# Kernel tuning notes

Measured on AMD Instinct MI355X. Metric: run time of the kernel, lower is better.

The kernel has to match this reference:

```python
import jax, jax.numpy as jnp
import numpy as np
import math

N, E = 50000, 800000
HID, EDIM, H = 128, 32, 8
D = HID // H            # head_dim = 16
FFN = 4 * HID           # ModelConstants.FFN_EXPANSION_FACTOR = 4
EPS = 1e-5


def layer_norm(x, g, b):
    mu = jnp.mean(x, axis=-1, keepdims=True)
    var = jnp.var(x, axis=-1, keepdims=True)
    return (x - mu) * jax.lax.rsqrt(var + EPS) * g + b


def setup_inputs() -> dict:
    key = jax.random.key(0)
    ks = jax.random.split(key, 16)
    s = 1.0 / math.sqrt(HID)
    inp = {
        "x": jax.random.normal(ks[0], (N, HID), jnp.float32),
        "edge_index": jax.random.randint(ks[1], (2, E), 0, N, jnp.int32),
        "edge_attr": jax.random.normal(ks[2], (E, EDIM), jnp.float32),
        # projections stored as (in, out): y = x @ W + b (same math as torch Linear)
        "qW": jax.random.normal(ks[3], (HID, HID), jnp.float32) * s,
        "qb": jnp.zeros((HID,), jnp.float32),
        "kW": jax.random.normal(ks[4], (HID, HID), jnp.float32) * s,
        "kb": jnp.zeros((HID,), jnp.float32),
        "vW": jax.random.normal(ks[5], (HID, HID), jnp.float32) * s,
        "vb": jnp.zeros((HID,), jnp.float32),
        "eW": jax.random.normal(ks[6], (EDIM, H), jnp.float32) / math.sqrt(EDIM),
        "eb": jnp.zeros((H,), jnp.float32),
        "oW": jax.random.normal(ks[7], (HID, HID), jnp.float32) * s,
        "ob": jnp.zeros((HID,), jnp.float32),
        "ln1_g": jnp.ones((HID,), jnp.float32),
        "ln1_b": jnp.zeros((HID,), jnp.float32),
        "f1W": jax.random.normal(ks[8], (HID, FFN), jnp.float32) * s,
        "f1b": jnp.zeros((FFN,), jnp.float32),
        "lnf_g": jnp.ones((FFN,), jnp.float32),
        "lnf_b": jnp.zeros((FFN,), jnp.float32),
        "f2W": jax.random.normal(ks[9], (FFN, HID), jnp.float32) / math.sqrt(FFN),
        "f2b": jnp.zeros((HID,), jnp.float32),
        "ln2_g": jnp.ones((HID,), jnp.float32),
        "ln2_b": jnp.zeros((HID,), jnp.float32),
    }
    return inp


def reference(x, edge_index, edge_attr, qW, qb, kW, kb, vW, vb, eW, eb, oW, ob,
              ln1_g, ln1_b, f1W, f1b, lnf_g, lnf_b, f2W, f2b, ln2_g, ln2_b):
    src, dst = edge_index[0], edge_index[1]
    q = (x @ qW + qb).reshape(N, H, D)
    k = (x @ kW + kb).reshape(N, H, D)
    v = (x @ vW + vb).reshape(N, H, D)
    edge_bias = edge_attr @ eW + eb                     # (E, H)
    # per-edge attention scores
    scores = jnp.sum(q[src] * k[dst], axis=-1) / math.sqrt(D) + edge_bias  # (E, H)
    # scatter softmax over edges grouped by dst
    mx = jax.ops.segment_max(scores, dst, num_segments=N)  # (N, H), -inf for empty
    mx = jnp.where(jnp.isinf(mx), jnp.zeros_like(mx), mx)
    ex = jnp.exp(scores - mx[dst])                      # (E, H)
    den = jax.ops.segment_sum(ex, dst, num_segments=N)
    den = jnp.maximum(den, 1e-8)
    attn = ex / den[dst]                                # (E, H)
    # weighted aggregation
    wv = v[src] * attn[:, :, None]                      # (E, H, D)
    out = jax.ops.segment_sum(wv, dst, num_segments=N)  # (N, H, D)
    out = out.reshape(N, HID) @ oW + ob
    x = layer_norm(x + out, ln1_g, ln1_b)
    h = x @ f1W + f1b
    h = jax.nn.gelu(layer_norm(h, lnf_g, lnf_b), approximate=False)
    h = h @ f2W + f2b
    x = layer_norm(x + h, ln2_g, ln2_b)
    return x
```

## Files before the change

### kernel.cpp

```cpp
#include <hip/hip_runtime.h>
#include <math.h>

#define LN_EPS 1e-5f

typedef __attribute__((ext_vector_type(8))) __bf16 bf16x8;
typedef __attribute__((ext_vector_type(4))) float f32x4;

__device__ inline float bf2f(unsigned short u) {
  union { unsigned int i; float f; } x; x.i = ((unsigned int)u) << 16; return x.f;
}
__device__ inline unsigned short f2bf(float f) {
  union { float f; unsigned int i; } x; x.f = f;
  unsigned int r = (x.i + 0x7FFFu + ((x.i >> 16) & 1u)) >> 16;
  return (unsigned short)r;
}
__device__ inline void gload_lds16(const void* g, void* l) {
  __builtin_amdgcn_global_load_lds((const __attribute__((address_space(1))) void*)g,
                                   (__attribute__((address_space(3))) void*)l, 16, 0, 0);
}

__global__ __launch_bounds__(256)
void to_bf16(const float* __restrict__ in, unsigned short* __restrict__ outp, long n) {
  long i = ((long)blockIdx.x * 256 + threadIdx.x) * 4;
  if (i >= n) return;
  float4 v = *(const float4*)&in[i];
  ushort4 o = { f2bf(v.x), f2bf(v.y), f2bf(v.z), f2bf(v.w) };
  *(ushort4*)&outp[i] = o;
}

__global__ __launch_bounds__(256)
void transpose_w(const float* __restrict__ W, unsigned short* __restrict__ Wt, int K, int M) {
  __shared__ float t[32][33];
  const int k0 = blockIdx.x * 32, m0 = blockIdx.y * 32;
  const int tx = threadIdx.x & 31, ty = threadIdx.x >> 5;
#pragma unroll
  for (int i = 0; i < 32; i += 8)
    t[ty + i][tx] = W[(size_t)(k0 + ty + i) * M + m0 + tx];
  __syncthreads();
#pragma unroll
  for (int i = 0; i < 32; i += 8)
    Wt[(size_t)(m0 + ty + i) * K + k0 + tx] = f2bf(t[tx][ty + i]);
}

__global__ __launch_bounds__(384)
void concat_bias3(const float* __restrict__ a, const float* __restrict__ b,
                  const float* __restrict__ c, float* __restrict__ o) {
  int t = threadIdx.x;
  o[t] = t < 128 ? a[t] : (t < 256 ? b[t - 128] : c[t - 256]);
}

template<bool OBF>
__global__ __launch_bounds__(256)
void gemm_mfma(const unsigned short* __restrict__ A, const unsigned short* __restrict__ Wt,
               const float* __restrict__ bias, void* __restrict__ Cout,
               int Nr, int K, int M) {
  __shared__ __align__(16) unsigned short As[128 * 64];
  __shared__ __align__(16) unsigned short Bs[128 * 64];
  const int tid = threadIdx.x;
  const int bm = blockIdx.x * 128, bn = blockIdx.y * 128;
  const int lane = tid & 63;
  const int wr = (tid >> 6) >> 1, wc = (tid >> 6) & 1;
  f32x4 acc[4][4] = {};
  const int nkt = K >> 6;
  for (int kt = 0; kt < nkt; ++kt) {
#pragma unroll
    for (int i = 0; i < 4; ++i) {
      int c = tid + i * 256;
      int row = c >> 3;
      int j = (c & 7) ^ (row & 7);
      int ar = bm + row; ar = ar < Nr ? ar : Nr - 1;
      gload_lds16(A + (size_t)ar * K + kt * 64 + j * 8, As + (size_t)c * 8);
      gload_lds16(Wt + (size_t)(bn + row) * K + kt * 64 + j * 8, Bs + (size_t)c * 8);
    }
    __syncthreads();
#pragma unroll
    for (int ks = 0; ks < 2; ++ks) {
      bf16x8 af[4], bfr[4];
#pragma unroll
      for (int f = 0; f < 4; ++f) {
        int rowa = wr * 64 + f * 16 + (lane & 15);
        int ja = (ks * 4 + (lane >> 4)) ^ (rowa & 7);
        af[f] = *(const bf16x8*)(As + rowa * 64 + ja * 8);
        int rowb = wc * 64 + f * 16 + (lane & 15);
        int jb = (ks * 4 + (lane >> 4)) ^ (rowb & 7);
        bfr[f] = *(const bf16x8*)(Bs + rowb * 64 + jb * 8);
      }
#pragma unroll
      for (int fr = 0; fr < 4; ++fr)
#pragma unroll
        for (int fc = 0; fc < 4; ++fc)
          acc[fr][fc] = __builtin_amdgcn_mfma_f32_16x16x32_bf16(af[fr], bfr[fc], acc[fr][fc], 0, 0, 0);
    }
    __syncthreads();
  }
#pragma unroll
  for (int fr = 0; fr < 4; ++fr) {
#pragma unroll
    for (int j = 0; j < 4; ++j) {
      int row = bm + wr * 64 + fr * 16 + (lane >> 4) * 4 + j;
      if (row < Nr) {
#pragma unroll
        for (int fc = 0; fc < 4; ++fc) {
          int col = bn + wc * 64 + fc * 16 + (lane & 15);
          float v = acc[fr][fc][j] + bias[col];
          if (OBF) ((unsigned short*)Cout)[(size_t)row * M + col] = f2bf(v);
          else     ((float*)Cout)[(size_t)row * M + col] = v;
        }
      }
    }
  }
}

template<bool WBF>
__global__ __launch_bounds__(256)
void gemm_ln(const unsigned short* __restrict__ A, const unsigned short* __restrict__ Wt,
             const float* __restrict__ bias, const float* __restrict__ res,
             const float* __restrict__ g, const float* __restrict__ b,
             float* __restrict__ y, unsigned short* __restrict__ ybf, int Nr, int K) {
  __shared__ __align__(16) unsigned short As[128 * 64];
  __shared__ __align__(16) unsigned short Bs[128 * 64];
  __shared__ float pls[128][2], plss[128][2];
  const int tid = threadIdx.x;
  const int bm = blockIdx.x * 128;
  const int lane = tid & 63;
  const int wr = (tid >> 6) >> 1, wc = (tid >> 6) & 1;
  f32x4 acc[4][4] = {};
  const int nkt = K >> 6;
  for (int kt = 0; kt < nkt; ++kt) {
#pragma unroll
    for (int i = 0; i < 4; ++i) {
      int c = tid + i * 256;
      int row = c >> 3;
      int j = (c & 7) ^ (row & 7);
      int ar = bm + row; ar = ar < Nr ? ar : Nr - 1;
      gload_lds16(A + (size_t)ar * K + kt * 64 + j * 8, As + (size_t)c * 8);
      gload_lds16(Wt + (size_t)row * K + kt * 64 + j * 8, Bs + (size_t)c * 8);
    }
    __syncthreads();
#pragma unroll
    for (int ks = 0; ks < 2; ++ks) {
      bf16x8 af[4], bfr[4];
#pragma unroll
      for (int f = 0; f < 4; ++f) {
        int rowa = wr * 64 + f * 16 + (lane & 15);
        int ja = (ks * 4 + (lane >> 4)) ^ (rowa & 7);
        af[f] = *(const bf16x8*)(As + rowa * 64 + ja * 8);
        int rowb = wc * 64 + f * 16 + (lane & 15);
        int jb = (ks * 4 + (lane >> 4)) ^ (rowb & 7);
        bfr[f] = *(const bf16x8*)(Bs + rowb * 64 + jb * 8);
      }
#pragma unroll
      for (int fr = 0; fr < 4; ++fr)
#pragma unroll
        for (int fc = 0; fc < 4; ++fc)
          acc[fr][fc] = __builtin_amdgcn_mfma_f32_16x16x32_bf16(af[fr], bfr[fc], acc[fr][fc], 0, 0, 0);
    }
    __syncthreads();
  }
#pragma unroll
  for (int fr = 0; fr < 4; ++fr) {
#pragma unroll
    for (int j = 0; j < 4; ++j) {
      const int rl = wr * 64 + fr * 16 + (lane >> 4) * 4 + j;
      const int row = bm + rl;
      const int rowc = row < Nr ? row : Nr - 1;
      float s = 0.f, ss = 0.f;
#pragma unroll
      for (int fc = 0; fc < 4; ++fc) {
        int col = wc * 64 + fc * 16 + (lane & 15);
        float val = acc[fr][fc][j] + bias[col] + res[(size_t)rowc * 128 + col];
        acc[fr][fc][j] = val;
        s += val; ss += val * val;
      }
      s += __shfl_xor(s, 1); ss += __shfl_xor(ss, 1);
      s += __shfl_xor(s, 2); ss += __shfl_xor(ss, 2);
      s += __shfl_xor(s, 4); ss += __shfl_xor(ss, 4);
      s += __shfl_xor(s, 8); ss += __shfl_xor(ss, 8);
      if ((lane & 15) == 0) { pls[rl][wc] = s; plss[rl][wc] = ss; }
    }
  }
  __syncthreads();
#pragma unroll
  for (int fr = 0; fr < 4; ++fr) {
#pragma unroll
    for (int j = 0; j < 4; ++j) {
      const int rl = wr * 64 + fr * 16 + (lane >> 4) * 4 + j;
      const int row = bm + rl;
      if (row >= Nr) continue;
      const float S = pls[rl][0] + pls[rl][1];
      const float SS = plss[rl][0] + plss[rl][1];
      const float mu = S * (1.f / 128.f);
      const float inv = rsqrtf(SS * (1.f / 128.f) - mu * mu + LN_EPS);
#pragma unroll
      for (int fc = 0; fc < 4; ++fc) {
        int col = wc * 64 + fc * 16 + (lane & 15);
        float o = (acc[fr][fc][j] - mu) * inv * g[col] + b[col];
        y[(size_t)row * 128 + col] = o;
        if (WBF) ybf[(size_t)row * 128 + col] = f2bf(o);
      }
    }
  }
}

__global__ __launch_bounds__(256)
void edge_hist(const int* __restrict__ ei, int* __restrict__ deg, int E) {
  int e = blockIdx.x * 256 + threadIdx.x;
  if (e < E) atomicAdd(&deg[ei[E + e]], 1);
}

__global__ __launch_bounds__(256)
void deg_block_sum(const int* __restrict__ deg, int* __restrict__ bsum, int N) {
  const int t = threadIdx.x;
  const int beg = blockIdx.x * 2048 + t * 8;
  int s = 0;
#pragma unroll
  for (int j = 0; j < 8; ++j) { int i = beg + j; if (i < N) s += deg[i]; }
#pragma unroll
  for (int off = 32; off; off >>= 1) s += __shfl_xor(s, off);
  __shared__ int ws[4];
  if ((t & 63) == 0) ws[t >> 6] = s;
  __syncthreads();
  if (t == 0) bsum[blockIdx.x] = ws[0] + ws[1] + ws[2] + ws[3];
}

__global__ __launch_bounds__(64)
void scan_bsum(int* __restrict__ bsum, int* __restrict__ offs_last, int nb) {
  const int t = threadIdx.x;
  int v = (t < nb) ? bsum[t] : 0;
  int inc = v;
#pragma unroll
  for (int off = 1; off < 64; off <<= 1) {
    int x = __shfl_up(inc, off);
    if (t >= off) inc += x;
  }
  if (t < nb) bsum[t] = inc - v;
  if (t == 63) *offs_last = inc;
}

__global__ __launch_bounds__(256)
void deg_scan_write(const int* __restrict__ deg, const int* __restrict__ bsum,
                    int* __restrict__ offs, int* __restrict__ pos, int N) {
  const int t = threadIdx.x;
  const int beg = blockIdx.x * 2048 + t * 8;
  int loc[8]; int T = 0;
#pragma unroll
  for (int j = 0; j < 8; ++j) { int i = beg + j; loc[j] = (i < N) ? deg[i] : 0; T += loc[j]; }
  int inc = T;
#pragma unroll
  for (int off = 1; off < 64; off <<= 1) {
    int x = __shfl_up(inc, off);
    if ((t & 63) >= off) inc += x;
  }
  __shared__ int ws[4];
  if ((t & 63) == 63) ws[t >> 6] = inc;
  __syncthreads();
  const int wid = t >> 6;
  int wbase = 0;
  for (int w = 0; w < wid; ++w) wbase += ws[w];
  int base = bsum[blockIdx.x] + wbase + inc - T;
#pragma unroll
  for (int j = 0; j < 8; ++j) {
    int i = beg + j;
    if (i < N) { offs[i] = base; pos[i] = base; base += loc[j]; }
  }
}

__global__ __launch_bounds__(256)
void edge_scatter_bias(const int* __restrict__ ei, int* __restrict__ pos,
                       const float* __restrict__ ea, const float* __restrict__ eW,
                       const float* __restrict__ eb, int* __restrict__ csr_src,
                       unsigned short* __restrict__ ebp, int E) {
  __shared__ float ews[256];
  __shared__ float ebs[8];
  const int tid = threadIdx.x;
  if (tid < 256) ews[tid] = eW[tid];
  if (tid < 8) ebs[tid] = eb[tid];
  __syncthreads();
  int e = blockIdx.x * 256 + tid;
  if (e >= E) return;
  float bias[8];
#pragma unroll
  for (int h = 0; h < 8; ++h) bias[h] = ebs[h];
#pragma unroll
  for (int i4 = 0; i4 < 8; ++i4) {
    float4 a = *(const float4*)&ea[(size_t)e * 32 + i4 * 4];
    float av[4] = {a.x, a.y, a.z, a.w};
#pragma unroll
    for (int j = 0; j < 4; ++j)
#pragma unroll
      for (int h = 0; h < 8; ++h) bias[h] += av[j] * ews[(i4 * 4 + j) * 8 + h];
  }
  int d = ei[E + e];
  int p = atomicAdd(&pos[d], 1);
  csr_src[p] = ei[e];
  union { unsigned short us[8]; uint4 v; } pk;
#pragma unroll
  for (int h = 0; h < 8; ++h) pk.us[h] = f2bf(bias[h]);
  *(uint4*)&ebp[(size_t)p * 8] = pk.v;
}

__global__ __launch_bounds__(256)
void node_agg(const int* __restrict__ csr_src, const int* __restrict__ offs,
              const unsigned short* __restrict__ qkv, const unsigned short* __restrict__ ebp,
              unsigned short* __restrict__ agg, int N) {
  const int wid = threadIdx.x >> 6, lane = threadIdx.x & 63;
  const int h = lane >> 3;
  const long n = (long)blockIdx.x * 4 + wid;
  if (n >= N) return;
  const int off = offs[n], end = offs[n + 1];
  const ushort2 kv2 = *(const ushort2*)&qkv[(size_t)n * 384 + 128 + lane * 2];
  const float k0 = bf2f(kv2.x), k1 = bf2f(kv2.y);
  float acc0 = 0.f, acc1 = 0.f, den = 0.f;
  int i = off;
  for (; i + 4 <= end; i += 4) {
    const size_t b0 = (size_t)csr_src[i] * 384;
    const size_t b1 = (size_t)csr_src[i + 1] * 384;
    const size_t b2 = (size_t)csr_src[i + 2] * 384;
    const size_t b3 = (size_t)csr_src[i + 3] * 384;
    const ushort2 qa = *(const ushort2*)&qkv[b0 + lane * 2];
    const ushort2 qb = *(const ushort2*)&qkv[b1 + lane * 2];
    const ushort2 qc = *(const ushort2*)&qkv[b2 + lane * 2];
    const ushort2 qd = *(const ushort2*)&qkv[b3 + lane * 2];
    const ushort2 va = *(const ushort2*)&qkv[b0 + 256 + lane * 2];
    const ushort2 vb = *(const ushort2*)&qkv[b1 + 256 + lane * 2];
    const ushort2 vc = *(const ushort2*)&qkv[b2 + 256 + lane * 2];
    const ushort2 vd = *(const ushort2*)&qkv[b3 + 256 + lane * 2];
    const float e0 = bf2f(ebp[(size_t)i * 8 + h]);
    const float e1 = bf2f(ebp[(size_t)(i + 1) * 8 + h]);
    const float e2 = bf2f(ebp[(size_t)(i + 2) * 8 + h]);
    const float e3 = bf2f(ebp[(size_t)(i + 3) * 8 + h]);
    float p0 = bf2f(qa.x) * k0 + bf2f(qa.y) * k1;
    float p1 = bf2f(qb.x) * k0 + bf2f(qb.y) * k1;
    float p2 = bf2f(qc.x) * k0 + bf2f(qc.y) * k1;
    float p3 = bf2f(qd.x) * k0 + bf2f(qd.y) * k1;
    p0 += __shfl_xor(p0, 1); p1 += __shfl_xor(p1, 1); p2 += __shfl_xor(p2, 1); p3 += __shfl_xor(p3, 1);
    p0 += __shfl_xor(p0, 2); p1 += __shfl_xor(p1, 2); p2 += __shfl_xor(p2, 2); p3 += __shfl_xor(p3, 2);
    p0 += __shfl_xor(p0, 4); p1 += __shfl_xor(p1, 4); p2 += __shfl_xor(p2, 4); p3 += __shfl_xor(p3, 4);
    const float x0 = __expf(p0 * 0.25f + e0);
    const float x1 = __expf(p1 * 0.25f + e1);
    const float x2 = __expf(p2 * 0.25f + e2);
    const float x3 = __expf(p3 * 0.25f + e3);
    den += (x0 + x1) + (x2 + x3);
    acc0 += bf2f(va.x) * x0 + bf2f(vb.x) * x1 + bf2f(vc.x) * x2 + bf2f(vd.x) * x3;
    acc1 += bf2f(va.y) * x0 + bf2f(vb.y) * x1 + bf2f(vc.y) * x2 + bf2f(vd.y) * x3;
  }
  for (; i < end; ++i) {
    const size_t b0 = (size_t)csr_src[i] * 384;
    const ushort2 qa = *(const ushort2*)&qkv[b0 + lane * 2];
    const ushort2 va = *(const ushort2*)&qkv[b0 + 256 + lane * 2];
    float p = bf2f(qa.x) * k0 + bf2f(qa.y) * k1;
    p += __shfl_xor(p, 1);
    p += __shfl_xor(p, 2);
    p += __shfl_xor(p, 4);
    const float ex = __expf(p * 0.25f + bf2f(ebp[(size_t)i * 8 + h]));
    den += ex;
    acc0 += bf2f(va.x) * ex;
    acc1 += bf2f(va.y) * ex;
  }
  const float r = 1.f / fmaxf(den, 1e-8f);
  ushort2 o; o.x = f2bf(acc0 * r); o.y = f2bf(acc1 * r);
  *(ushort2*)&agg[(size_t)n * 128 + lane * 2] = o;
}

__global__ __launch_bounds__(256)
void ln_gelu512(unsigned short* __restrict__ hbuf, const float* __restrict__ g,
                const float* __restrict__ b, int Nr) {
  __shared__ float rs[4], rss[4];
  const long row = blockIdx.x;
  const int tid = threadIdx.x;
  ushort2 u = *(ushort2*)&hbuf[row * 512 + tid * 2];
  float v0 = bf2f(u.x), v1 = bf2f(u.y);
  float s = v0 + v1, ss = v0 * v0 + v1 * v1;
#pragma unroll
  for (int off = 32; off; off >>= 1) { s += __shfl_xor(s, off); ss += __shfl_xor(ss, off); }
  const int wid = tid >> 6, lane = tid & 63;
  if (lane == 0) { rs[wid] = s; rss[wid] = ss; }
  __syncthreads();
  s = rs[0] + rs[1] + rs[2] + rs[3];
  ss = rss[0] + rss[1] + rss[2] + rss[3];
  const float mu = s * (1.f / 512.f);
  const float inv = rsqrtf(ss * (1.f / 512.f) - mu * mu + LN_EPS);
  float t0 = (v0 - mu) * inv * g[tid * 2] + b[tid * 2];
  float t1 = (v1 - mu) * inv * g[tid * 2 + 1] + b[tid * 2 + 1];
  t0 = 0.5f * t0 * (1.f + erff(t0 * 0.70710678118654752f));
  t1 = 0.5f * t1 * (1.f + erff(t1 * 0.70710678118654752f));
  ushort2 o; o.x = f2bf(t0); o.y = f2bf(t1);
  *(ushort2*)&hbuf[row * 512 + tid * 2] = o;
}

extern "C" void kernel_launch(void* const* d_in, const int* in_sizes, int n_in,
                              void* d_out, int out_size, void* d_ws, size_t ws_size,
                              hipStream_t stream) {
  const float* x   = (const float*)d_in[0];
  const int*   ei  = (const int*)d_in[1];
  const float* ea  = (const float*)d_in[2];
  const float* qW  = (const float*)d_in[3];
  const float* qbi = (const float*)d_in[4];
  const float* kW  = (const float*)d_in[5];
  const float* kbi = (const float*)d_in[6];
  const float* vW  = (const float*)d_in[7];
  const float* vbi = (const float*)d_in[8];
  const float* eW  = (const float*)d_in[9];
  const float* eb  = (const float*)d_in[10];
  const float* oW  = (const float*)d_in[11];
  const float* ob  = (const float*)d_in[12];
  const float* ln1_g = (const float*)d_in[13];
  const float* ln1_b = (const float*)d_in[14];
  const float* f1W = (const float*)d_in[15];
  const float* f1b = (const float*)d_in[16];
  const float* lnf_g = (const float*)d_in[17];
  const float* lnf_b = (const float*)d_in[18];
  const float* f2W = (const float*)d_in[19];
  const float* f2b = (const float*)d_in[20];
  const float* ln2_g = (const float*)d_in[21];
  const float* ln2_b = (const float*)d_in[22];
  float* out = (float*)d_out;

  const int N = in_sizes[0] / 128;
  const int E = in_sizes[1] / 2;
  const size_t NH = (size_t)N * 128;

  float* F = (float*)d_ws;
  unsigned short* xbf   = (unsigned short*)F;
  unsigned short* qkvb  = (unsigned short*)(F + NH / 2);
  unsigned short* ebp   = (unsigned short*)(F + 2 * NH);
  unsigned short* aggb  = (unsigned short*)(F + 2 * NH + NH / 2);
  float*          x1    = F + 3 * NH;
  unsigned short* x1bf  = xbf;
  unsigned short* hbufb = (unsigned short*)(F + NH / 2);
  int* ib      = (int*)(F + 4 * NH);
  int* csr_src = ib;
  int* offs    = ib + E;
  int* pos     = ib + E + N + 1;
  int* bsum    = ib + E + 2 * N + 1;
  unsigned short* wt = (unsigned short*)(ib + E + 2 * N + 128);
  unsigned short* qkvWt = wt;
  unsigned short* oWt   = wt + 49152;
  unsigned short* f1Wt  = wt + 65536;
  unsigned short* f2Wt  = wt + 131072;
  float* qkvbias = (float*)(wt + 196608);

  dim3 blk(256);
  dim3 gqkv((N + 127) / 128, 3);
  dim3 g128((N + 127) / 128, 1);
  dim3 gf1((N + 127) / 128, 4);
  const int nb = (N + 2047) / 2048;

  to_bf16<<<dim3((int)((NH / 4 + 255) / 256)), blk, 0, stream>>>(x, xbf, (long)NH);
  transpose_w<<<dim3(4, 4), blk, 0, stream>>>(qW, qkvWt, 128, 128);
  transpose_w<<<dim3(4, 4), blk, 0, stream>>>(kW, qkvWt + 16384, 128, 128);
  transpose_w<<<dim3(4, 4), blk, 0, stream>>>(vW, qkvWt + 32768, 128, 128);
  transpose_w<<<dim3(4, 4), blk, 0, stream>>>(oW, oWt, 128, 128);
  transpose_w<<<dim3(4, 16), blk, 0, stream>>>(f1W, f1Wt, 128, 512);
  transpose_w<<<dim3(16, 4), blk, 0, stream>>>(f2W, f2Wt, 512, 128);
  concat_bias3<<<dim3(1), dim3(384), 0, stream>>>(qbi, kbi, vbi, qkvbias);

  gemm_mfma<true><<<gqkv, blk, 0, stream>>>(xbf, qkvWt, qkvbias, qkvb, N, 128, 384);

  hipMemsetAsync(pos, 0, (size_t)N * sizeof(int), stream);
  edge_hist<<<dim3((E + 255) / 256), blk, 0, stream>>>(ei, pos, E);
  deg_block_sum<<<dim3(nb), blk, 0, stream>>>(pos, bsum, N);
  scan_bsum<<<dim3(1), dim3(64), 0, stream>>>(bsum, offs + N, nb);
  deg_scan_write<<<dim3(nb), blk, 0, stream>>>(pos, bsum, offs, pos, N);
  edge_scatter_bias<<<dim3((E + 255) / 256), blk, 0, stream>>>(ei, pos, ea, eW, eb,
                                                               csr_src, ebp, E);

  node_agg<<<dim3((N + 3) / 4), blk, 0, stream>>>(csr_src, offs, qkvb, ebp, aggb, N);

  gemm_ln<true><<<g128, blk, 0, stream>>>(aggb, oWt, ob, x, ln1_g, ln1_b, x1, x1bf, N, 128);

  gemm_mfma<true><<<gf1, blk, 0, stream>>>(x1bf, f1Wt, f1b, hbufb, N, 128, 512);
  ln_gelu512<<<dim3(N), blk, 0, stream>>>(hbufb, lnf_g, lnf_b, N);
  gemm_ln<false><<<g128, blk, 0, stream>>>(hbufb, f2Wt, f2b, x1, ln2_g, ln2_b, out, nullptr, N, 512);
}
```

Before: 339.8 us.

## Merge weight prep kernels, drop fp32 LN1 output, deepen node_agg unroll

```diff
diff --git a/kernel.cpp b/kernel.cpp
--- a/kernel.cpp
+++ b/kernel.cpp
@@ -28,25 +28,39 @@
   *(ushort4*)&outp[i] = o;
 }
 
-__global__ __launch_bounds__(256)
-void transpose_w(const float* __restrict__ W, unsigned short* __restrict__ Wt, int K, int M) {
-  __shared__ float t[32][33];
-  const int k0 = blockIdx.x * 32, m0 = blockIdx.y * 32;
+struct WDesc { const float* W; unsigned short* Wt; int K, M, ntx; };
+__global__ __launch_bounds__(256)
+void prep_weights(const float* qW, const float* kW, const float* vW, const float* oW,
+                  const float* f1W, const float* f2W,
+                  unsigned short* qkvWt, unsigned short* oWt,
+                  unsigned short* f1Wt, unsigned short* f2Wt,
+                  const float* qb, const float* kb, const float* vb, float* qkvbias) {
+  const int t = blockIdx.x;
+  if (t == 192) {
+    int i = threadIdx.x;
+    if (i < 128) { qkvbias[i] = qb[i]; qkvbias[128 + i] = kb[i]; }
+    else if (i < 256) qkvbias[256 + (i - 128)] = vb[i - 128];
+    return;
+  }
+  const float* W; unsigned short* Wt; int K, M, lt;
+  if (t < 64)       { K = 128; M = 128; lt = t & 15;
+    if (t < 16)      { W = qW; Wt = qkvWt; }
+    else if (t < 32) { W = kW; Wt = qkvWt + 16384; }
+    else if (t < 48) { W = vW; Wt = qkvWt + 32768; }
+    else             { W = oW; Wt = oWt; } }
+  else if (t < 128) { K = 128; M = 512; lt = t - 64; W = f1W; Wt = f1Wt; }
+  else              { K = 512; M = 128; lt = t - 128; W = f2W; Wt = f2Wt; }
+  const int ktiles = K >> 5;
+  const int k0 = (lt % ktiles) * 32, m0 = (lt / ktiles) * 32;
+  __shared__ float tb[32][33];
   const int tx = threadIdx.x & 31, ty = threadIdx.x >> 5;
 #pragma unroll
   for (int i = 0; i < 32; i += 8)
-    t[ty + i][tx] = W[(size_t)(k0 + ty + i) * M + m0 + tx];
+    tb[ty + i][tx] = W[(size_t)(k0 + ty + i) * M + m0 + tx];
   __syncthreads();
 #pragma unroll
   for (int i = 0; i < 32; i += 8)
-    Wt[(size_t)(m0 + ty + i) * K + k0 + tx] = f2bf(t[tx][ty + i]);
-}
-
-__global__ __launch_bounds__(384)
-void concat_bias3(const float* __restrict__ a, const float* __restrict__ b,
-                  const float* __restrict__ c, float* __restrict__ o) {
-  int t = threadIdx.x;
-  o[t] = t < 128 ? a[t] : (t < 256 ? b[t - 128] : c[t - 256]);
+    Wt[(size_t)(m0 + ty + i) * K + k0 + tx] = f2bf(tb[tx][ty + i]);
 }
 
 template<bool OBF>
@@ -111,10 +125,10 @@
   }
 }
 
-template<bool WBF>
+template<bool WF32, bool WBF, bool RESBF>
 __global__ __launch_bounds__(256)
 void gemm_ln(const unsigned short* __restrict__ A, const unsigned short* __restrict__ Wt,
-             const float* __restrict__ bias, const float* __restrict__ res,
+             const float* __restrict__ bias, const void* __restrict__ res,
              const float* __restrict__ g, const float* __restrict__ b,
              float* __restrict__ y, unsigned short* __restrict__ ybf, int Nr, int K) {
   __shared__ __align__(16) unsigned short As[128 * 64];
@@ -168,7 +182,9 @@
 #pragma unroll
       for (int fc = 0; fc < 4; ++fc) {
         int col = wc * 64 + fc * 16 + (lane & 15);
-        float val = acc[fr][fc][j] + bias[col] + res[(size_t)rowc * 128 + col];
+        float rv = RESBF ? bf2f(((const unsigned short*)res)[(size_t)rowc * 128 + col])
+                         : ((const float*)res)[(size_t)rowc * 128 + col];
+        float val = acc[fr][fc][j] + bias[col] + rv;
         acc[fr][fc][j] = val;
         s += val; ss += val * val;
       }
@@ -195,8 +211,8 @@
       for (int fc = 0; fc < 4; ++fc) {
         int col = wc * 64 + fc * 16 + (lane & 15);
         float o = (acc[fr][fc][j] - mu) * inv * g[col] + b[col];
-        y[(size_t)row * 128 + col] = o;
-        if (WBF) ybf[(size_t)row * 128 + col] = f2bf(o);
+        if (WF32) y[(size_t)row * 128 + col] = o;
+        if (WBF)  ybf[(size_t)row * 128 + col] = f2bf(o);
       }
     }
   }
@@ -312,37 +328,63 @@
   const float k0 = bf2f(kv2.x), k1 = bf2f(kv2.y);
   float acc0 = 0.f, acc1 = 0.f, den = 0.f;
   int i = off;
+  for (; i + 8 <= end; i += 8) {
+    size_t bb[8];
+#pragma unroll
+    for (int u = 0; u < 8; ++u) bb[u] = (size_t)csr_src[i + u] * 384;
+    ushort2 qv[8], vv[8];
+#pragma unroll
+    for (int u = 0; u < 8; ++u) qv[u] = *(const ushort2*)&qkv[bb[u] + lane * 2];
+#pragma unroll
+    for (int u = 0; u < 8; ++u) vv[u] = *(const ushort2*)&qkv[bb[u] + 256 + lane * 2];
+    float ebv[8];
+#pragma unroll
+    for (int u = 0; u < 8; ++u) ebv[u] = bf2f(ebp[(size_t)(i + u) * 8 + h]);
+    float p[8];
+#pragma unroll
+    for (int u = 0; u < 8; ++u) p[u] = bf2f(qv[u].x) * k0 + bf2f(qv[u].y) * k1;
+#pragma unroll
+    for (int u = 0; u < 8; ++u) {
+      p[u] += __shfl_xor(p[u], 1);
+      p[u] += __shfl_xor(p[u], 2);
+      p[u] += __shfl_xor(p[u], 4);
+    }
+#pragma unroll
+    for (int u = 0; u < 8; ++u) {
+      const float ex = __expf(p[u] * 0.25f + ebv[u]);
+      den += ex;
+      acc0 += bf2f(vv[u].x) * ex;
+      acc1 += bf2f(vv[u].y) * ex;
+    }
+  }
   for (; i + 4 <= end; i += 4) {
-    const size_t b0 = (size_t)csr_src[i] * 384;
-    const size_t b1 = (size_t)csr_src[i + 1] * 384;
-    const size_t b2 = (size_t)csr_src[i + 2] * 384;
-    const size_t b3 = (size_t)csr_src[i + 3] * 384;
-    const ushort2 qa = *(const ushort2*)&qkv[b0 + lane * 2];
-    const ushort2 qb = *(const ushort2*)&qkv[b1 + lane * 2];
-    const ushort2 qc = *(const ushort2*)&qkv[b2 + lane * 2];
-    const ushort2 qd = *(const ushort2*)&qkv[b3 + lane * 2];
-    const ushort2 va = *(const ushort2*)&qkv[b0 + 256 + lane * 2];
-    const ushort2 vb = *(const ushort2*)&qkv[b1 + 256 + lane * 2];
-    const ushort2 vc = *(const ushort2*)&qkv[b2 + 256 + lane * 2];
-    const ushort2 vd = *(const ushort2*)&qkv[b3 + 256 + lane * 2];
-    const float e0 = bf2f(ebp[(size_t)i * 8 + h]);
-    const float e1 = bf2f(ebp[(size_t)(i + 1) * 8 + h]);
-    const float e2 = bf2f(ebp[(size_t)(i + 2) * 8 + h]);
-    const float e3 = bf2f(ebp[(size_t)(i + 3) * 8 + h]);
-    float p0 = bf2f(qa.x) * k0 + bf2f(qa.y) * k1;
-    float p1 = bf2f(qb.x) * k0 + bf2f(qb.y) * k1;
-    float p2 = bf2f(qc.x) * k0 + bf2f(qc.y) * k1;
-    float p3 = bf2f(qd.x) * k0 + bf2f(qd.y) * k1;
-    p0 += __shfl_xor(p0, 1); p1 += __shfl_xor(p1, 1); p2 += __shfl_xor(p2, 1); p3 += __shfl_xor(p3, 1);
-    p0 += __shfl_xor(p0, 2); p1 += __shfl_xor(p1, 2); p2 += __shfl_xor(p2, 2); p3 += __shfl_xor(p3, 2);
-    p0 += __shfl_xor(p0, 4); p1 += __shfl_xor(p1, 4); p2 += __shfl_xor(p2, 4); p3 += __shfl_xor(p3, 4);
-    const float x0 = __expf(p0 * 0.25f + e0);
-    const float x1 = __expf(p1 * 0.25f + e1);
-    const float x2 = __expf(p2 * 0.25f + e2);
-    const float x3 = __expf(p3 * 0.25f + e3);
-    den += (x0 + x1) + (x2 + x3);
-    acc0 += bf2f(va.x) * x0 + bf2f(vb.x) * x1 + bf2f(vc.x) * x2 + bf2f(vd.x) * x3;
-    acc1 += bf2f(va.y) * x0 + bf2f(vb.y) * x1 + bf2f(vc.y) * x2 + bf2f(vd.y) * x3;
+    size_t bb[4];
+#pragma unroll
+    for (int u = 0; u < 4; ++u) bb[u] = (size_t)csr_src[i + u] * 384;
+    ushort2 qv[4], vv[4];
+#pragma unroll
+    for (int u = 0; u < 4; ++u) qv[u] = *(const ushort2*)&qkv[bb[u] + lane * 2];
+#pragma unroll
+    for (int u = 0; u < 4; ++u) vv[u] = *(const ushort2*)&qkv[bb[u] + 256 + lane * 2];
+    float ebv[4];
+#pragma unroll
+    for (int u = 0; u < 4; ++u) ebv[u] = bf2f(ebp[(size_t)(i + u) * 8 + h]);
+    float p[4];
+#pragma unroll
+    for (int u = 0; u < 4; ++u) p[u] = bf2f(qv[u].x) * k0 + bf2f(qv[u].y) * k1;
+#pragma unroll
+    for (int u = 0; u < 4; ++u) {
+      p[u] += __shfl_xor(p[u], 1);
+      p[u] += __shfl_xor(p[u], 2);
+      p[u] += __shfl_xor(p[u], 4);
+    }
+#pragma unroll
+    for (int u = 0; u < 4; ++u) {
+      const float ex = __expf(p[u] * 0.25f + ebv[u]);
+      den += ex;
+      acc0 += bf2f(vv[u].x) * ex;
+      acc1 += bf2f(vv[u].y) * ex;
+    }
   }
   for (; i < end; ++i) {
     const size_t b0 = (size_t)csr_src[i] * 384;
@@ -425,7 +467,6 @@
   unsigned short* qkvb  = (unsigned short*)(F + NH / 2);
   unsigned short* ebp   = (unsigned short*)(F + 2 * NH);
   unsigned short* aggb  = (unsigned short*)(F + 2 * NH + NH / 2);
-  float*          x1    = F + 3 * NH;
   unsigned short* x1bf  = xbf;
   unsigned short* hbufb = (unsigned short*)(F + NH / 2);
   int* ib      = (int*)(F + 4 * NH);
@@ -445,31 +486,29 @@
   dim3 g128((N + 127) / 128, 1);
   dim3 gf1((N + 127) / 128, 4);
   const int nb = (N + 2047) / 2048;
+  const int ge = (E + 255) / 256;
 
   to_bf16<<<dim3((int)((NH / 4 + 255) / 256)), blk, 0, stream>>>(x, xbf, (long)NH);
-  transpose_w<<<dim3(4, 4), blk, 0, stream>>>(qW, qkvWt, 128, 128);
-  transpose_w<<<dim3(4, 4), blk, 0, stream>>>(kW, qkvWt + 16384, 128, 128);
-  transpose_w<<<dim3(4, 4), blk, 0, stream>>>(vW, qkvWt + 32768, 128, 128);
-  transpose_w<<<dim3(4, 4), blk, 0, stream>>>(oW, oWt, 128, 128);
-  transpose_w<<<dim3(4, 16), blk, 0, stream>>>(f1W, f1Wt, 128, 512);
-  transpose_w<<<dim3(16, 4), blk, 0, stream>>>(f2W, f2Wt, 512, 128);
-  concat_bias3<<<dim3(1), dim3(384), 0, stream>>>(qbi, kbi, vbi, qkvbias);
+  prep_weights<<<dim3(193), blk, 0, stream>>>(qW, kW, vW, oW, f1W, f2W,
+                                              qkvWt, oWt, f1Wt, f2Wt,
+                                              qbi, kbi, vbi, qkvbias);
 
   gemm_mfma<true><<<gqkv, blk, 0, stream>>>(xbf, qkvWt, qkvbias, qkvb, N, 128, 384);
 
   hipMemsetAsync(pos, 0, (size_t)N * sizeof(int), stream);
-  edge_hist<<<dim3((E + 255) / 256), blk, 0, stream>>>(ei, pos, E);
+  edge_hist<<<dim3(ge), blk, 0, stream>>>(ei, pos, E);
   deg_block_sum<<<dim3(nb), blk, 0, stream>>>(pos, bsum, N);
   scan_bsum<<<dim3(1), dim3(64), 0, stream>>>(bsum, offs + N, nb);
   deg_scan_write<<<dim3(nb), blk, 0, stream>>>(pos, bsum, offs, pos, N);
-  edge_scatter_bias<<<dim3((E + 255) / 256), blk, 0, stream>>>(ei, pos, ea, eW, eb,
-                                                               csr_src, ebp, E);
+  edge_scatter_bias<<<dim3(ge), blk, 0, stream>>>(ei, pos, ea, eW, eb, csr_src, ebp, E);
 
   node_agg<<<dim3((N + 3) / 4), blk, 0, stream>>>(csr_src, offs, qkvb, ebp, aggb, N);
 
-  gemm_ln<true><<<g128, blk, 0, stream>>>(aggb, oWt, ob, x, ln1_g, ln1_b, x1, x1bf, N, 128);
+  gemm_ln<false, true, false><<<g128, blk, 0, stream>>>(aggb, oWt, ob, x,
+                                                        ln1_g, ln1_b, nullptr, x1bf, N, 128);
 
   gemm_mfma<true><<<gf1, blk, 0, stream>>>(x1bf, f1Wt, f1b, hbufb, N, 128, 512);
   ln_gelu512<<<dim3(N), blk, 0, stream>>>(hbufb, lnf_g, lnf_b, N);
-  gemm_ln<false><<<g128, blk, 0, stream>>>(hbufb, f2Wt, f2b, x1, ln2_g, ln2_b, out, nullptr, N, 512);
-}
+  gemm_ln<true, false, true><<<g128, blk, 0, stream>>>(hbufb, f2Wt, f2b, x1bf,
+                                                       ln2_g, ln2_b, out, nullptr, N, 512);
+}
```

Result: faster. 315.6 us (-7.1%).
